# Optimization experiments

Hardware: AMD Instinct MI355X
Metric: run time of the kernel (lower is better)

## Reference

```python
import jax, jax.numpy as jnp
import numpy as np

B, P, NOBJ = 16, 19248, 32
NUM_CLASSES = 81  # 80 foreground + background (code uses num_classes+1 w/o focal loss)
POS_TH, NEG_TH = 0.5, 0.4
VAR0, VAR1 = 0.1, 0.2  # standard SSD encode variances
NEGPOS_RATIO = 3


def setup_inputs() -> dict:
    key = jax.random.key(0)
    k1, k2, k3, k4, k5 = jax.random.split(key, 5)
    loc_data = jax.random.normal(k1, (B, P, 4), jnp.float32)
    conf_data = jax.random.normal(k2, (B, P, NUM_CLASSES), jnp.float32)
    # priors in (cx, cy, w, h), normalized coords
    pc = jax.random.uniform(k3, (P, 2), jnp.float32, 0.05, 0.95)
    pw = jax.random.uniform(jax.random.fold_in(k3, 1), (P, 2), jnp.float32, 0.05, 0.4)
    priors = jnp.concatenate([pc, pw], -1)
    # gt boxes in point form (xmin, ymin, xmax, ymax)
    gc = jax.random.uniform(k4, (B, NOBJ, 2), jnp.float32, 0.2, 0.8)
    gw = jax.random.uniform(jax.random.fold_in(k4, 1), (B, NOBJ, 2), jnp.float32, 0.05, 0.3)
    gt_boxes = jnp.concatenate([gc - gw / 2, gc + gw / 2], -1)
    gt_labels = jax.random.randint(k5, (B, NOBJ), 0, NUM_CLASSES - 1)  # 0..79
    return {"loc_data": loc_data, "conf_data": conf_data, "priors": priors,
            "gt_boxes": gt_boxes, "gt_labels": gt_labels}


def _point_form(p):
    # (cx,cy,w,h) -> (xmin,ymin,xmax,ymax)
    return jnp.concatenate([p[..., :2] - p[..., 2:] / 2, p[..., :2] + p[..., 2:] / 2], -1)


def _jaccard(a, b):
    # a: [N,4], b: [P,4] point form -> IoU [N,P]
    lt = jnp.maximum(a[:, None, :2], b[None, :, :2])
    rb = jnp.minimum(a[:, None, 2:], b[None, :, 2:])
    wh = jnp.clip(rb - lt, 0.0)
    inter = wh[..., 0] * wh[..., 1]
    area_a = (a[:, 2] - a[:, 0]) * (a[:, 3] - a[:, 1])
    area_b = (b[:, 2] - b[:, 0]) * (b[:, 3] - b[:, 1])
    return inter / (area_a[:, None] + area_b[None, :] - inter)


def _match_one(gt, labels, priors_pf, priors):
    # SSD match: per-prior best gt + force each gt's best prior to be positive
    ov = _jaccard(gt, priors_pf)                 # [N,P]
    best_prior_idx = jnp.argmax(ov, axis=1)      # [N]
    best_truth_ov = jnp.max(ov, axis=0)          # [P]
    best_truth_idx = jnp.argmax(ov, axis=0)      # [P]
    best_truth_ov = best_truth_ov.at[best_prior_idx].set(2.0)
    best_truth_idx = best_truth_idx.at[best_prior_idx].set(jnp.arange(gt.shape[0]))
    matched = gt[best_truth_idx]                 # [P,4] point form
    conf = labels[best_truth_idx] + 1
    conf = jnp.where(best_truth_ov < POS_TH, -1, conf)   # neutral band
    conf = jnp.where(best_truth_ov < NEG_TH, 0, conf)    # background
    # encode offsets with variances
    m_cxcy = (matched[:, :2] + matched[:, 2:]) / 2
    m_wh = matched[:, 2:] - matched[:, :2]
    g_cxcy = (m_cxcy - priors[:, :2]) / (VAR0 * priors[:, 2:])
    g_wh = jnp.log(m_wh / priors[:, 2:]) / VAR1
    return jnp.concatenate([g_cxcy, g_wh], -1), conf


def reference(loc_data, conf_data, priors, gt_boxes, gt_labels):
    priors_pf = _point_form(priors)
    loc_t, conf_t = jax.vmap(lambda g, l: _match_one(g, l, priors_pf, priors))(gt_boxes, gt_labels)
    loc_t = jax.lax.stop_gradient(loc_t)
    pos = conf_t > 0                                   # [B,P]
    n_pos = pos.sum(axis=1)                            # [B]
    N = jnp.maximum(pos.sum(), 1).astype(loc_data.dtype)
    # localization: smooth L1 over positives
    d = loc_data - loc_t
    ad = jnp.abs(d)
    sl1 = jnp.where(ad < 1.0, 0.5 * d * d, ad - 0.5)
    loss_l = jnp.sum(sl1 * pos[..., None])
    # confidence: hard negative mining at 3:1
    logp = jax.nn.log_softmax(conf_data, axis=-1)      # [B,P,C]
    ct = jnp.maximum(conf_t, 0)
    nll = -jnp.take_along_axis(logp, ct[..., None], axis=-1)[..., 0]  # [B,P]
    mine = jnp.where(pos | (conf_t < 0), 0.0, nll)     # exclude pos & neutral from mining
    rank = jnp.argsort(jnp.argsort(-mine, axis=1), axis=1)
    num_neg = jnp.minimum(NEGPOS_RATIO * n_pos, P - 1)
    neg = (rank < num_neg[:, None]) & (conf_t == 0)
    loss_c = jnp.sum(nll * (pos | neg))
    return jnp.stack([loss_l, loss_c]) / N
```

## Files before the change

kernel.cpp:

```cpp
#include <hip/hip_runtime.h>
#include <cstdint>
#include <cstddef>

#define BB 16
#define PP 19248
#define NOBJ 32
#define NCLS 81
#define POS_TH 0.5f
#define NEG_TH 0.4f
#define VAR0 0.1f
#define VAR1 0.2f
#define NEGPOS 3

#define MTB 256
#define NMB ((PP + MTB - 1) / MTB)
#define MAINB 1024
#define ROWS_PB 64
#define NSLOT ((PP + ROWS_PB - 1) / ROWS_PB)
#define ST 1024

__global__ __launch_bounds__(MTB) void k_match(const float* __restrict__ priors,
                                               const float* __restrict__ gt_boxes,
                                               unsigned long long* __restrict__ gkey,
                                               float* __restrict__ bto,
                                               int* __restrict__ bti) {
    const int b = blockIdx.y;
    const int p = blockIdx.x * MTB + threadIdx.x;
    const int wid = threadIdx.x >> 6, lane = threadIdx.x & 63;
    __shared__ float4 sg[NOBJ];
    __shared__ unsigned long long wkey[4][NOBJ];
    if (threadIdx.x < NOBJ) sg[threadIdx.x] = ((const float4*)gt_boxes)[b * NOBJ + threadIdx.x];
    __syncthreads();

    const bool valid = p < PP;
    float px1 = 0.f, py1 = 0.f, px2 = 0.f, py2 = 0.f, parea = 0.f;
    if (valid) {
        float4 pr = ((const float4*)priors)[p];
        float hw = pr.z / 2.0f, hh = pr.w / 2.0f;
        px1 = pr.x - hw; py1 = pr.y - hh; px2 = pr.x + hw; py2 = pr.y + hh;
        parea = (px2 - px1) * (py2 - py1);
    }

    float best = -1.0f;
    int bn = 0;
    for (int n = 0; n < NOBJ; ++n) {
        float4 g = sg[n];
        float iou = -1.0f;
        if (valid) {
            {
#pragma clang fp contract(off)
                float ix1 = fmaxf(g.x, px1), iy1 = fmaxf(g.y, py1);
                float ix2 = fminf(g.z, px2), iy2 = fminf(g.w, py2);
                float iw = fmaxf(ix2 - ix1, 0.0f), ih = fmaxf(iy2 - iy1, 0.0f);
                float inter = iw * ih;
                float garea = (g.z - g.x) * (g.w - g.y);
                iou = inter / (garea + parea - inter);
            }
        }
        if (iou > best) { best = iou; bn = n; }

        float m = iou;
        m = fmaxf(m, __shfl_xor(m, 1, 64));
        m = fmaxf(m, __shfl_xor(m, 2, 64));
        m = fmaxf(m, __shfl_xor(m, 4, 64));
        m = fmaxf(m, __shfl_xor(m, 8, 64));
        m = fmaxf(m, __shfl_xor(m, 16, 64));
        m = fmaxf(m, __shfl_xor(m, 32, 64));
        unsigned long long ball = __ballot(iou == m);
        if (lane == 0) {
            unsigned long long key = 0ull;
            if (m >= 0.0f) {
                unsigned psrc = (unsigned)(blockIdx.x * MTB + wid * 64 +
                                           (int)__builtin_ctzll(ball));
                key = (((unsigned long long)__float_as_uint(m)) << 32) |
                      (unsigned long long)(0xFFFFFFFFu - psrc);
            }
            wkey[wid][n] = key;
        }
    }

    if (valid) {
        bto[(size_t)b * PP + p] = best;
        bti[(size_t)b * PP + p] = bn;
    }
    __syncthreads();
    if (threadIdx.x < NOBJ) {
        unsigned long long k0 = wkey[0][threadIdx.x];
        unsigned long long k1 = wkey[1][threadIdx.x];
        unsigned long long k2 = wkey[2][threadIdx.x];
        unsigned long long k3 = wkey[3][threadIdx.x];
        if (k1 > k0) k0 = k1;
        if (k2 > k0) k0 = k2;
        if (k3 > k0) k0 = k3;
        atomicMax(&gkey[b * NOBJ + threadIdx.x], k0);
    }
}

__device__ __forceinline__ float sl1(float d) {
    float ad = fabsf(d);
    return ad < 1.0f ? 0.5f * d * d : ad - 0.5f;
}

__global__ __launch_bounds__(MAINB, 8) void k_main(const float* __restrict__ loc_data,
                                                   const float* __restrict__ conf_data,
                                                   const float* __restrict__ priors,
                                                   const float* __restrict__ gt_boxes,
                                                   const int* __restrict__ gt_labels,
                                                   const float* __restrict__ bto,
                                                   const int* __restrict__ bti,
                                                   const unsigned long long* __restrict__ gkey,
                                                   float* __restrict__ mine,
                                                   float* __restrict__ p_ll,
                                                   float* __restrict__ p_lc,
                                                   int* __restrict__ p_np) {
    const int b = blockIdx.y;
    const int t = threadIdx.x;
    const int wid = t >> 6;
    const int lane = t & 63;
    const int g = lane >> 4;
    const int j = lane & 15;
    const int rbase = blockIdx.x * ROWS_PB + wid * 4;
    const int r = rbase + g;
    const bool valid = r < PP;

    unsigned pst = 0xFFFFFFFFu;
    if (lane < NOBJ) {
        unsigned long long key = gkey[b * NOBJ + lane];
        pst = 0xFFFFFFFFu - (unsigned)(key & 0xFFFFFFFFull);
    }

    const float* rowp = conf_data + ((size_t)b * PP + r) * NCLS;
    float s = 0.0f;
    if (valid) {
        s  = __expf(rowp[j]);
        s += __expf(rowp[j + 16]);
        s += __expf(rowp[j + 32]);
        s += __expf(rowp[j + 48]);
        s += __expf(rowp[j + 64]);
        if (j == 0) s += __expf(rowp[80]);
    }
    s += __shfl_xor(s, 1, 64);
    s += __shfl_xor(s, 2, 64);
    s += __shfl_xor(s, 4, 64);
    s += __shfl_xor(s, 8, 64);
    const float lse = __logf(s);

    unsigned long long b0 = __ballot(pst == (unsigned)(rbase + 0));
    unsigned long long b1 = __ballot(pst == (unsigned)(rbase + 1));
    unsigned long long b2 = __ballot(pst == (unsigned)(rbase + 2));
    unsigned long long b3 = __ballot(pst == (unsigned)(rbase + 3));
    unsigned long long mball = (g == 0) ? b0 : (g == 1) ? b1 : (g == 2) ? b2 : b3;

    float my_ll = 0.0f, my_lc = 0.0f;
    int my_pos = 0;

    if (valid && j == 0) {
        const size_t idx = (size_t)b * PP + r;
        float ov = bto[idx];
        int ti = bti[idx];
        if (mball) { ov = 2.0f; ti = 63 - __builtin_clzll(mball); }
        int conf_c = gt_labels[b * NOBJ + ti] + 1;
        if (ov < POS_TH) conf_c = -1;
        if (ov < NEG_TH) conf_c = 0;
        const int ct = conf_c > 0 ? conf_c : 0;
        const float nll = lse - rowp[ct];

        if (conf_c > 0) {
            my_pos = 1;
            my_lc = nll;
            float4 gbox = ((const float4*)gt_boxes)[b * NOBJ + ti];
            float4 pr = ((const float4*)priors)[r];
            float mcx = (gbox.x + gbox.z) / 2.0f, mcy = (gbox.y + gbox.w) / 2.0f;
            float mw = gbox.z - gbox.x, mh = gbox.w - gbox.y;
            float t0 = (mcx - pr.x) / (VAR0 * pr.z);
            float t1 = (mcy - pr.y) / (VAR0 * pr.w);
            float t2 = logf(mw / pr.z) / VAR1;
            float t3 = logf(mh / pr.w) / VAR1;
            float4 ld = ((const float4*)loc_data)[(size_t)b * PP + r];
            my_ll = sl1(ld.x - t0) + sl1(ld.y - t1) + sl1(ld.z - t2) + sl1(ld.w - t3);
        }
        mine[idx] = (conf_c == 0) ? nll : 0.0f;
    }

    for (int off = 32; off > 0; off >>= 1) {
        my_ll += __shfl_down(my_ll, off, 64);
        my_lc += __shfl_down(my_lc, off, 64);
        my_pos += __shfl_down(my_pos, off, 64);
    }
    __shared__ float rll[16], rlc[16];
    __shared__ int rnp[16];
    if (lane == 0) { rll[wid] = my_ll; rlc[wid] = my_lc; rnp[wid] = my_pos; }
    __syncthreads();
    if (t == 0) {
        float a = 0.0f, c = 0.0f;
        int n = 0;
#pragma unroll
        for (int w = 0; w < 16; ++w) { a += rll[w]; c += rlc[w]; n += rnp[w]; }
        p_ll[b * NSLOT + blockIdx.x] = a;
        p_lc[b * NSLOT + blockIdx.x] = c;
        p_np[b * NSLOT + blockIdx.x] = n;
    }
}

__global__ __launch_bounds__(ST) void k_select(const float* __restrict__ mine,
                                               const float* __restrict__ p_ll,
                                               const float* __restrict__ p_lc,
                                               const int* __restrict__ p_np,
                                               float* __restrict__ acc,
                                               int* __restrict__ acc_np,
                                               unsigned* __restrict__ done,
                                               float* __restrict__ out) {
    const int b = blockIdx.x;
    const int tid = threadIdx.x;
    const int wid = tid >> 6, lane = tid & 63;
    constexpr int NW = ST / 64;

    float ll = 0.0f, lc = 0.0f;
    int np = 0;
    for (int i = tid; i < NSLOT; i += ST) {
        ll += p_ll[b * NSLOT + i];
        lc += p_lc[b * NSLOT + i];
        np += p_np[b * NSLOT + i];
    }
    for (int off = 32; off > 0; off >>= 1) {
        ll += __shfl_down(ll, off, 64);
        lc += __shfl_down(lc, off, 64);
        np += __shfl_down(np, off, 64);
    }
    __shared__ float rll[NW], rlc[NW];
    __shared__ int rnp[NW];
    __shared__ float s_ll, s_lc;
    __shared__ int s_np;
    if (lane == 0) { rll[wid] = ll; rlc[wid] = lc; rnp[wid] = np; }
    __syncthreads();
    if (tid == 0) {
        float a = 0.0f, c = 0.0f;
        int n = 0;
        for (int w = 0; w < NW; ++w) { a += rll[w]; c += rlc[w]; n += rnp[w]; }
        s_ll = a; s_lc = c; s_np = n;
    }
    __syncthreads();
    const int np_b = s_np;
    const int k = min(NEGPOS * np_b, PP - 1);
    float neg = 0.0f;

    const float* mv = mine + (size_t)b * PP;
    if (k > 0) {
        __shared__ unsigned swh[NW * 16];
        __shared__ unsigned stot[16];
        __shared__ unsigned s_prefix;
        __shared__ int s_rem;
        __shared__ float s_neg;
        if (tid == 0) { s_prefix = 0u; s_rem = k; }
        __syncthreads();

        for (int pass = 0; pass < 8; ++pass) {
            const int shift = 28 - 4 * pass;
            const unsigned hm = (pass == 0) ? 0u : (0xFFFFFFFFu << (shift + 4));
            const unsigned prefix = s_prefix;

            unsigned cnt[16];
#pragma unroll
            for (int v = 0; v < 16; ++v) cnt[v] = 0u;

            for (int i = tid; i < PP; i += ST) {
                unsigned bits = __float_as_uint(mv[i]);
                unsigned key = ((bits & hm) == prefix) ? ((bits >> shift) & 15u) : 16u;
                if (__any(key != 16u)) {
#pragma unroll
                    for (int v = 0; v < 16; ++v)
                        cnt[v] += (unsigned)__popcll(__ballot(key == (unsigned)v));
                }
            }
            if (lane == 0) {
#pragma unroll
                for (int v = 0; v < 16; ++v) swh[wid * 16 + v] = cnt[v];
            }
            __syncthreads();
            if (tid < 16) {
                unsigned tt = 0;
#pragma unroll
                for (int w = 0; w < NW; ++w) tt += swh[w * 16 + tid];
                stot[tid] = tt;
            }
            __syncthreads();
            if (tid == 0) {
                int rem = s_rem;
                unsigned cum = 0;
                int chosen = 0;
                for (int v = 15; v >= 0; --v) {
                    unsigned c = stot[v];
                    if (cum + c >= (unsigned)rem) { chosen = v; s_rem = rem - (int)cum; break; }
                    cum += c;
                }
                s_prefix = prefix | ((unsigned)chosen << shift);
            }
            __syncthreads();
        }

        const unsigned T = s_prefix;
        float sum = 0.0f;
        unsigned cnt = 0;
        for (int i = tid; i < PP; i += ST) {
            float v = mv[i];
            if (__float_as_uint(v) > T) { sum += v; cnt++; }
        }
        for (int off = 32; off > 0; off >>= 1) {
            sum += __shfl_down(sum, off, 64);
            cnt += __shfl_down(cnt, off, 64);
        }
        __shared__ float rs[NW];
        __shared__ unsigned rc[NW];
        if (lane == 0) { rs[wid] = sum; rc[wid] = cnt; }
        __syncthreads();
        if (tid == 0) {
            float S = 0.0f;
            int G = 0;
            for (int w = 0; w < NW; ++w) { S += rs[w]; G += (int)rc[w]; }
            s_neg = S + (float)(k - G) * __uint_as_float(T);
        }
        __syncthreads();
        neg = s_neg;
    }

    if (tid == 0) {
        atomicAdd(&acc[0], s_ll);
        atomicAdd(&acc[1], s_lc + neg);
        atomicAdd(acc_np, np_b);
        __threadfence();
        unsigned prev = atomicAdd(done, 1u);
        if (prev == BB - 1) {
            int tp = atomicAdd(acc_np, 0);
            float N = (float)max(tp, 1);
            float a0 = atomicAdd(&acc[0], 0.0f);
            float a1 = atomicAdd(&acc[1], 0.0f);
            out[0] = a0 / N;
            out[1] = a1 / N;
        }
    }
}

extern "C" void kernel_launch(void* const* d_in, const int* in_sizes, int n_in,
                              void* d_out, int out_size, void* d_ws, size_t ws_size,
                              hipStream_t stream) {
    const float* loc    = (const float*)d_in[0];
    const float* conf   = (const float*)d_in[1];
    const float* priors = (const float*)d_in[2];
    const float* gt     = (const float*)d_in[3];
    const int*   labels = (const int*)d_in[4];
    float* out = (float*)d_out;

    char* ws = (char*)d_ws;
    const size_t SZ_BP = (size_t)BB * PP * 4;
    const size_t SZ_SLOT = (size_t)BB * NSLOT * 4;
    unsigned long long* gkey = (unsigned long long*)ws;
    float*    acc    = (float*)   (ws + 4096);
    int*      acc_np = (int*)     (ws + 4104);
    unsigned* done   = (unsigned*)(ws + 4108);
    float* bto  = (float*)(ws + 4224);
    int*   bti  = (int*)  (ws + 4224 + SZ_BP);
    float* mine = (float*)(ws + 4224 + 2 * SZ_BP);
    float* p_ll = (float*)(ws + 4224 + 3 * SZ_BP);
    float* p_lc = (float*)(ws + 4224 + 3 * SZ_BP + SZ_SLOT);
    int*   p_np = (int*)  (ws + 4224 + 3 * SZ_BP + 2 * SZ_SLOT);

    (void)hipMemsetAsync(ws, 0, 4224, stream);

    dim3 mg(NMB, BB);
    k_match<<<mg, MTB, 0, stream>>>(priors, gt, gkey, bto, bti);

    dim3 kg(NSLOT, BB);
    k_main<<<kg, MAINB, 0, stream>>>(loc, conf, priors, gt, labels, bto, bti, gkey,
                                     mine, p_ll, p_lc, p_np);

    k_select<<<BB, ST, 0, stream>>>(mine, p_ll, p_lc, p_np, acc, acc_np, done, out);
}
```

Measured before the change: 257.0 us.

## Replace 8-pass radix select with shared-memory histogram plus candidate-bin refinement

The k_select kernel's top-k threshold search previously made eight full passes over each batch row of mining losses, using ballot-based 4-bit histograms. It now builds a single 8192-bin shared-memory histogram on the top 13 bits and locates the bin holding the k-th value with a hierarchical prefix scan. One more pass sums values above that bin and gathers the bin's members into a compact buffer. The remaining low bits are resolved by radix passes over that small buffer only. A fallback keeps the old path for when the boundary bin overflows, at the cost of shared-memory atomics that can contend when many values share a bin (e.g. zeros).

```diff
diff --git a/kernel.cpp b/kernel.cpp
--- a/kernel.cpp
+++ b/kernel.cpp
@@ -18,6 +18,11 @@
 #define ROWS_PB 64
 #define NSLOT ((PP + ROWS_PB - 1) / ROWS_PB)
 #define ST 1024
+
+#define HSHIFT 19
+#define HSIZE 8192
+#define HPT (HSIZE / ST)
+#define CAP HSIZE
 
 __global__ __launch_bounds__(MTB) void k_match(const float* __restrict__ priors,
                                                const float* __restrict__ gt_boxes,
@@ -215,6 +220,21 @@
     const int wid = tid >> 6, lane = tid & 63;
     constexpr int NW = ST / 64;
 
+    __shared__ unsigned hist[HSIZE];
+    __shared__ unsigned s_tsum[ST];
+    __shared__ unsigned s_wsum[NW];
+    __shared__ float rll[NW], rlc[NW];
+    __shared__ int rnp[NW];
+    __shared__ float rs1[NW], rs2[NW];
+    __shared__ unsigned rc2[NW];
+    __shared__ float s_ll, s_lc, s_neg;
+    __shared__ int s_np, s_B, s_G1;
+    __shared__ unsigned s_cntB, s_cnt, s_prefix;
+    __shared__ int s_rem;
+    __shared__ unsigned h16[16];
+    __shared__ unsigned swh[NW * 16];
+    __shared__ unsigned stot[16];
+
     float ll = 0.0f, lc = 0.0f;
     int np = 0;
     for (int i = tid; i < NSLOT; i += ST) {
@@ -227,10 +247,6 @@
         lc += __shfl_down(lc, off, 64);
         np += __shfl_down(np, off, 64);
     }
-    __shared__ float rll[NW], rlc[NW];
-    __shared__ int rnp[NW];
-    __shared__ float s_ll, s_lc;
-    __shared__ int s_np;
     if (lane == 0) { rll[wid] = ll; rlc[wid] = lc; rnp[wid] = np; }
     __syncthreads();
     if (tid == 0) {
@@ -238,94 +254,208 @@
         int n = 0;
         for (int w = 0; w < NW; ++w) { a += rll[w]; c += rlc[w]; n += rnp[w]; }
         s_ll = a; s_lc = c; s_np = n;
+        s_neg = 0.0f;
     }
     __syncthreads();
     const int np_b = s_np;
     const int k = min(NEGPOS * np_b, PP - 1);
-    float neg = 0.0f;
 
     const float* mv = mine + (size_t)b * PP;
+    const float4* mv4 = (const float4*)mv;
+    constexpr int PP4 = PP / 4;
+
     if (k > 0) {
-        __shared__ unsigned swh[NW * 16];
-        __shared__ unsigned stot[16];
-        __shared__ unsigned s_prefix;
-        __shared__ int s_rem;
-        __shared__ float s_neg;
-        if (tid == 0) { s_prefix = 0u; s_rem = k; }
+        for (int i = tid; i < HSIZE; i += ST) hist[i] = 0u;
         __syncthreads();
-
-        for (int pass = 0; pass < 8; ++pass) {
-            const int shift = 28 - 4 * pass;
-            const unsigned hm = (pass == 0) ? 0u : (0xFFFFFFFFu << (shift + 4));
-            const unsigned prefix = s_prefix;
-
-            unsigned cnt[16];
+        for (int i = tid; i < PP4; i += ST) {
+            float4 v = mv4[i];
+            atomicAdd(&hist[__float_as_uint(v.x) >> HSHIFT], 1u);
+            atomicAdd(&hist[__float_as_uint(v.y) >> HSHIFT], 1u);
+            atomicAdd(&hist[__float_as_uint(v.z) >> HSHIFT], 1u);
+            atomicAdd(&hist[__float_as_uint(v.w) >> HSHIFT], 1u);
+        }
+        __syncthreads();
+
+        unsigned tsum = 0;
+        const int hb = tid * HPT;
 #pragma unroll
-            for (int v = 0; v < 16; ++v) cnt[v] = 0u;
-
-            for (int i = tid; i < PP; i += ST) {
-                unsigned bits = __float_as_uint(mv[i]);
-                unsigned key = ((bits & hm) == prefix) ? ((bits >> shift) & 15u) : 16u;
-                if (__any(key != 16u)) {
-#pragma unroll
-                    for (int v = 0; v < 16; ++v)
-                        cnt[v] += (unsigned)__popcll(__ballot(key == (unsigned)v));
-                }
-            }
-            if (lane == 0) {
-#pragma unroll
-                for (int v = 0; v < 16; ++v) swh[wid * 16 + v] = cnt[v];
-            }
-            __syncthreads();
-            if (tid < 16) {
-                unsigned tt = 0;
-#pragma unroll
-                for (int w = 0; w < NW; ++w) tt += swh[w * 16 + tid];
-                stot[tid] = tt;
-            }
-            __syncthreads();
-            if (tid == 0) {
-                int rem = s_rem;
-                unsigned cum = 0;
-                int chosen = 0;
-                for (int v = 15; v >= 0; --v) {
-                    unsigned c = stot[v];
-                    if (cum + c >= (unsigned)rem) { chosen = v; s_rem = rem - (int)cum; break; }
-                    cum += c;
-                }
-                s_prefix = prefix | ((unsigned)chosen << shift);
-            }
-            __syncthreads();
-        }
-
-        const unsigned T = s_prefix;
-        float sum = 0.0f;
-        unsigned cnt = 0;
-        for (int i = tid; i < PP; i += ST) {
-            float v = mv[i];
-            if (__float_as_uint(v) > T) { sum += v; cnt++; }
-        }
-        for (int off = 32; off > 0; off >>= 1) {
-            sum += __shfl_down(sum, off, 64);
-            cnt += __shfl_down(cnt, off, 64);
-        }
-        __shared__ float rs[NW];
-        __shared__ unsigned rc[NW];
-        if (lane == 0) { rs[wid] = sum; rc[wid] = cnt; }
+        for (int v = 0; v < HPT; ++v) tsum += hist[hb + v];
+        s_tsum[tid] = tsum;
+        unsigned wsum = tsum;
+        for (int off = 32; off > 0; off >>= 1) wsum += __shfl_down(wsum, off, 64);
+        if (lane == 0) s_wsum[wid] = wsum;
         __syncthreads();
         if (tid == 0) {
-            float S = 0.0f;
-            int G = 0;
-            for (int w = 0; w < NW; ++w) { S += rs[w]; G += (int)rc[w]; }
-            s_neg = S + (float)(k - G) * __uint_as_float(T);
+            unsigned cum = 0;
+            int w = NW - 1;
+            for (; w > 0; --w) {
+                if (cum + s_wsum[w] >= (unsigned)k) break;
+                cum += s_wsum[w];
+            }
+            int t = (w + 1) * 64 - 1;
+            for (; t > w * 64; --t) {
+                if (cum + s_tsum[t] >= (unsigned)k) break;
+                cum += s_tsum[t];
+            }
+            int bin = t * HPT + HPT - 1;
+            for (; bin > t * HPT; --bin) {
+                if (cum + hist[bin] >= (unsigned)k) break;
+                cum += hist[bin];
+            }
+            s_B = bin;
+            s_G1 = (int)cum;
+            s_cntB = hist[bin];
+            s_cnt = 0u;
         }
         __syncthreads();
-        neg = s_neg;
+        const int B = s_B;
+        const int r = k - s_G1;
+        const unsigned cntB = s_cntB;
+        const unsigned bin_lo = (unsigned)B << HSHIFT;
+        const unsigned hi_base = (unsigned)(B + 1) << HSHIFT;
+        unsigned* cbuf = hist;
+
+        if (cntB <= CAP) {
+            float S1 = 0.0f;
+            for (int i = tid; i < PP4; i += ST) {
+                float4 v = mv4[i];
+                unsigned bx = __float_as_uint(v.x);
+                unsigned by = __float_as_uint(v.y);
+                unsigned bz = __float_as_uint(v.z);
+                unsigned bw = __float_as_uint(v.w);
+                if (bx >= hi_base) S1 += v.x;
+                else if (bx >= bin_lo) cbuf[atomicAdd(&s_cnt, 1u)] = bx;
+                if (by >= hi_base) S1 += v.y;
+                else if (by >= bin_lo) cbuf[atomicAdd(&s_cnt, 1u)] = by;
+                if (bz >= hi_base) S1 += v.z;
+                else if (bz >= bin_lo) cbuf[atomicAdd(&s_cnt, 1u)] = bz;
+                if (bw >= hi_base) S1 += v.w;
+                else if (bw >= bin_lo) cbuf[atomicAdd(&s_cnt, 1u)] = bw;
+            }
+            for (int off = 32; off > 0; off >>= 1) S1 += __shfl_down(S1, off, 64);
+            if (lane == 0) rs1[wid] = S1;
+            __syncthreads();
+
+            if (tid == 0) { s_prefix = bin_lo; s_rem = r; }
+            __syncthreads();
+            for (int pass = 0; pass < 5; ++pass) {
+                const int shift = (pass < 4) ? (15 - 4 * pass) : 0;
+                const int width = (pass < 4) ? 4 : 3;
+                const int nb = 1 << width;
+                const unsigned hm = 0xFFFFFFFFu << (shift + width);
+                if (tid < 16) h16[tid] = 0u;
+                __syncthreads();
+                const unsigned prefix = s_prefix;
+                for (unsigned i = tid; i < cntB; i += ST) {
+                    unsigned bits = cbuf[i];
+                    if ((bits & hm) == prefix)
+                        atomicAdd(&h16[(bits >> shift) & (nb - 1)], 1u);
+                }
+                __syncthreads();
+                if (tid == 0) {
+                    int rem = s_rem;
+                    unsigned cum = 0;
+                    int chosen = 0;
+                    for (int v = nb - 1; v >= 0; --v) {
+                        unsigned c = h16[v];
+                        if (cum + c >= (unsigned)rem) { chosen = v; s_rem = rem - (int)cum; break; }
+                        cum += c;
+                    }
+                    s_prefix = prefix | ((unsigned)chosen << shift);
+                }
+                __syncthreads();
+            }
+            const unsigned T = s_prefix;
+
+            float S2 = 0.0f;
+            unsigned c2 = 0;
+            for (unsigned i = tid; i < cntB; i += ST) {
+                unsigned bits = cbuf[i];
+                if (bits > T) { S2 += __uint_as_float(bits); c2++; }
+            }
+            for (int off = 32; off > 0; off >>= 1) {
+                S2 += __shfl_down(S2, off, 64);
+                c2 += __shfl_down(c2, off, 64);
+            }
+            if (lane == 0) { rs2[wid] = S2; rc2[wid] = c2; }
+            __syncthreads();
+            if (tid == 0) {
+                float S1t = 0.0f, S2t = 0.0f;
+                unsigned c2t = 0;
+                for (int w = 0; w < NW; ++w) { S1t += rs1[w]; S2t += rs2[w]; c2t += rc2[w]; }
+                s_neg = S1t + S2t + (float)(r - (int)c2t) * __uint_as_float(T);
+            }
+            __syncthreads();
+        } else {
+            if (tid == 0) { s_prefix = 0u; s_rem = k; }
+            __syncthreads();
+            for (int pass = 0; pass < 8; ++pass) {
+                const int shift = 28 - 4 * pass;
+                const unsigned hm = (pass == 0) ? 0u : (0xFFFFFFFFu << (shift + 4));
+                const unsigned prefix = s_prefix;
+                unsigned cnt[16];
+#pragma unroll
+                for (int v = 0; v < 16; ++v) cnt[v] = 0u;
+                for (int i = tid; i < PP; i += ST) {
+                    unsigned bits = __float_as_uint(mv[i]);
+                    unsigned key = ((bits & hm) == prefix) ? ((bits >> shift) & 15u) : 16u;
+                    if (__any(key != 16u)) {
+#pragma unroll
+                        for (int v = 0; v < 16; ++v)
+                            cnt[v] += (unsigned)__popcll(__ballot(key == (unsigned)v));
+                    }
+                }
+                if (lane == 0) {
+#pragma unroll
+                    for (int v = 0; v < 16; ++v) swh[wid * 16 + v] = cnt[v];
+                }
+                __syncthreads();
+                if (tid < 16) {
+                    unsigned tt = 0;
+#pragma unroll
+                    for (int w = 0; w < NW; ++w) tt += swh[w * 16 + tid];
+                    stot[tid] = tt;
+                }
+                __syncthreads();
+                if (tid == 0) {
+                    int rem = s_rem;
+                    unsigned cum = 0;
+                    int chosen = 0;
+                    for (int v = 15; v >= 0; --v) {
+                        unsigned c = stot[v];
+                        if (cum + c >= (unsigned)rem) { chosen = v; s_rem = rem - (int)cum; break; }
+                        cum += c;
+                    }
+                    s_prefix = prefix | ((unsigned)chosen << shift);
+                }
+                __syncthreads();
+            }
+            const unsigned T = s_prefix;
+            float sum = 0.0f;
+            unsigned cnt = 0;
+            for (int i = tid; i < PP; i += ST) {
+                float v = mv[i];
+                if (__float_as_uint(v) > T) { sum += v; cnt++; }
+            }
+            for (int off = 32; off > 0; off >>= 1) {
+                sum += __shfl_down(sum, off, 64);
+                cnt += __shfl_down(cnt, off, 64);
+            }
+            if (lane == 0) { rs2[wid] = sum; rc2[wid] = cnt; }
+            __syncthreads();
+            if (tid == 0) {
+                float S = 0.0f;
+                int G = 0;
+                for (int w = 0; w < NW; ++w) { S += rs2[w]; G += (int)rc2[w]; }
+                s_neg = S + (float)(k - G) * __uint_as_float(T);
+            }
+            __syncthreads();
+        }
     }
 
     if (tid == 0) {
         atomicAdd(&acc[0], s_ll);
-        atomicAdd(&acc[1], s_lc + neg);
+        atomicAdd(&acc[1], s_lc + s_neg);
         atomicAdd(acc_np, np_b);
         __threadfence();
         unsigned prev = atomicAdd(done, 1u);
```

After: 211.8 us. 17.6% less time.
